# Optimization experiments

Measured on AMD Instinct MI355X. Metric: run time of the kernel, lower is better.

Reference implementation:

```python
import jax, jax.numpy as jnp
import numpy as np

CUTOFF = 5.0
MAX_NBR = 32      # max_num_neighbors
LOOP = True
B, M = 128, 1024  # molecules, atoms per molecule (batch is uniform: batch[i] = i // M)
BOX = 26.0        # box side chosen so ~30 atoms fall within CUTOFF


def setup_inputs() -> dict:
    key = jax.random.key(0)
    pos = jax.random.uniform(key, (B * M, 3), dtype=jnp.float32) * BOX
    batch = jnp.repeat(jnp.arange(B, dtype=jnp.int32), M)
    return {"pos": pos, "batch": batch}


def reference(pos, batch):
    # radius_graph with per-graph (molecule) candidate search. Equal-size
    # molecules (batch = arange // M) let us use a dense [B, M, M] candidate
    # matrix per molecule; truncation keeps the K nearest within cutoff
    # (PyG keeps an arbitrary K within cutoff; nearest-K is the deterministic
    # variant). Output has fixed shape [2, B*M*K] padded with self-loops.
    posb = pos.reshape(B, M, 3)
    sq = jnp.sum(posb * posb, axis=-1)                       # [B, M]
    dot = jnp.einsum('bmd,bnd->bmn', posb, posb)             # [B, M, M]
    d2 = jnp.maximum(sq[:, :, None] + sq[:, None, :] - 2.0 * dot, 0.0)
    within = d2 <= CUTOFF * CUTOFF
    if not LOOP:
        within = within & ~jnp.eye(M, dtype=bool)[None]
    neg = jnp.where(within, -d2, -jnp.inf)
    vals, idx = jax.lax.top_k(neg, MAX_NBR)                  # [B, M, K]
    valid = jnp.isfinite(vals)
    center = jnp.arange(M, dtype=idx.dtype)[None, :, None]   # [1, M, 1]
    idx_eff = jnp.where(valid, idx, center)                  # pad invalid -> self

    b_ix = jnp.arange(B)[:, None, None]
    nbr = posb[b_ix, idx_eff]                                # [B, M, K, 3]
    edge_vec = nbr - posb[:, :, None, :]                     # pos[src] - pos[dst]

    is_self = idx_eff == center
    wmask = valid & ~is_self                                 # self-loops get weight 0
    d2sel = jnp.sum(edge_vec * edge_vec, axis=-1)
    edge_weight = jnp.where(wmask, jnp.sqrt(jnp.where(wmask, d2sel, 1.0)), 0.0)

    offs = (jnp.arange(B, dtype=idx.dtype) * M)[:, None, None]
    src = (offs + idx_eff).reshape(-1)                       # neighbor (edge_index[0])
    dst = jnp.broadcast_to(offs + center, (B, M, MAX_NBR)).reshape(-1)
    edge_index = jnp.stack([src, dst])                       # [2, B*M*K]
    return edge_index, edge_weight.reshape(-1), edge_vec.reshape(-1, 3)
```

## Files before the change

kernel.cpp:

```cpp
#include <hip/hip_runtime.h>

#define NB 128
#define NM 1024
#define NK 32
#define NS 12
#define CUT2 25.0f
#define CUT2_BITS 0x41C80000u
#define KEYMASK   0xFFFFFC00u
#define INV_CELL  (1.0f/5.2f)
#define NCELL3    125

typedef unsigned int   u32;
typedef unsigned short u16;
typedef float vf4 __attribute__((ext_vector_type(4)));

__global__ __launch_bounds__(256) void pack_bin(const float* __restrict__ pos,
                                                float4* __restrict__ sortedg,
                                                u16* __restrict__ origid,
                                                u16* __restrict__ startsg)
{
  __shared__ u32 hist[NCELL3 + 1];
  __shared__ u32 starts[NCELL3 + 1];
  __shared__ u32 cur[NCELL3];
  const int tid = threadIdx.x;
  const int mb  = blockIdx.x;
  if (tid <= NCELL3) hist[tid] = 0;
  __syncthreads();

  float xx[4], yy[4], zz[4];
  int cid[4];
#pragma unroll
  for (int k = 0; k < 4; ++k) {
    int i  = k * 256 + tid;
    int gi = mb * NM + i;
    float x = pos[3*gi+0], y = pos[3*gi+1], z = pos[3*gi+2];
    xx[k] = x; yy[k] = y; zz[k] = z;
    int cx = (int)(x * INV_CELL); cx = cx > 4 ? 4 : cx;
    int cy = (int)(y * INV_CELL); cy = cy > 4 ? 4 : cy;
    int cz = (int)(z * INV_CELL); cz = cz > 4 ? 4 : cz;
    cid[k] = (cz * 5 + cy) * 5 + cx;
    atomicAdd(&hist[cid[k]], 1u);
  }
  __syncthreads();
  if (tid == 0) {
    u32 run = 0;
    for (int i = 0; i < NCELL3; ++i) { starts[i] = run; run += hist[i]; }
    starts[NCELL3] = run;
  }
  __syncthreads();
  if (tid <= NCELL3) startsg[mb*(NCELL3+1) + tid] = (u16)starts[tid];
  if (tid <  NCELL3) cur[tid] = starts[tid];
  __syncthreads();
#pragma unroll
  for (int k = 0; k < 4; ++k) {
    int i = k * 256 + tid;
    u32 p = atomicAdd(&cur[cid[k]], 1u);
    float x = xx[k], y = yy[k], z = zz[k];
    sortedg[mb*NM + p] = make_float4(-2.f*x, -2.f*y, -2.f*z, x*x + y*y + z*z);
    origid[mb*NM + p]  = (u16)i;
  }
}

__device__ __forceinline__ void ce_asc(u32 &a, u32 &b) {
  u32 mn = a < b ? a : b;
  u32 mx = a < b ? b : a;
  a = mn; b = mx;
}

template <int N, int K, int D>
__device__ __forceinline__ void bitonic_pass(u32* r) {
#pragma unroll
  for (int i = 0; i < N; ++i)
    if ((i & D) == 0) {
      if ((i & K) == 0) ce_asc(r[i], r[i | D]);
      else              ce_asc(r[i | D], r[i]);
    }
}

__global__ __launch_bounds__(256, 8) void radius_knn(const float4* __restrict__ sortedg,
                                                     const u16* __restrict__ origg,
                                                     const u16* __restrict__ startsg,
                                                     float* __restrict__ out)
{
  __shared__ u32 lmem[4096];
  __shared__ u16 orig_s[NM];
  u16* lists  = (u16*)lmem;
  u32* rowbuf = lmem + 1536;
  u16* flat   = (u16*)(lmem + 1568);
  u16* st_s   = (u16*)(lmem + 2112);

  const int tid     = threadIdx.x;
  const int ctr     = tid & 63;
  const int quarter = tid >> 6;
  const int molb    = blockIdx.x & 127;
  const int grp     = blockIdx.x >> 7;
  const int spos    = grp * 64 + ctr;
  const int molbase = molb * NM;

  for (int t = tid; t < NM; t += 256) orig_s[t] = origg[molbase + t];
  if (tid <= NCELL3) st_s[tid] = startsg[molb*(NCELL3+1) + tid];

  const float4 mc  = sortedg[molbase + spos];
  const int   mloc = origg[molbase + spos];
  const float mex = -0.5f*mc.x, mey = -0.5f*mc.y, mez = -0.5f*mc.z;
  const float mew = mc.w;
  const int c = molbase + mloc;

  int cx = (int)(mex * INV_CELL); cx = cx > 4 ? 4 : cx;
  int cy = (int)(mey * INV_CELL); cy = cy > 4 ? 4 : cy;
  int cz = (int)(mez * INV_CELL); cz = cz > 4 ? 4 : cz;
  int mnx = cx, mxx = cx, mny = cy, mxy = cy, mnz = cz, mxz = cz;
#pragma unroll
  for (int m = 32; m; m >>= 1) {
    mnx = min(mnx, __shfl_xor(mnx, m, 64)); mxx = max(mxx, __shfl_xor(mxx, m, 64));
    mny = min(mny, __shfl_xor(mny, m, 64)); mxy = max(mxy, __shfl_xor(mxy, m, 64));
    mnz = min(mnz, __shfl_xor(mnz, m, 64)); mxz = max(mxz, __shfl_xor(mxz, m, 64));
  }
  __syncthreads();

  if (quarter == 0) {
    const int zlo = max(mnz-1, 0), zhi = min(mxz+1, 4);
    const int ylo = max(mny-1, 0), yhi = min(mxy+1, 4);
    const int xlo = max(mnx-1, 0), xhi = min(mxx+1, 4);
    const int rz = ctr / 5, ry = ctr % 5;
    int czc = zlo + rz, cyc = ylo + ry;
    u32 rs = 0, len = 0;
    if (ctr < 25 && czc <= zhi && cyc <= yhi) {
      int rowb = (czc*5 + cyc)*5;
      rs  = st_s[rowb + xlo];
      u32 re = st_s[rowb + xhi + 1];
      len = re - rs;
    }
    u32 incl = len;
#pragma unroll
    for (int d = 1; d < 32; d <<= 1) {
      u32 t = __shfl_up(incl, d, 64);
      if (ctr >= d) incl += t;
    }
    if (ctr < 25)  rowbuf[ctr] = (rs << 16) | (incl - len);
    if (ctr == 24) { rowbuf[25] = incl; lmem[1563] = incl; }
  }
  __syncthreads();

  const int C  = (int)lmem[1563];
  const int C4 = (C + 15) & ~15;
  for (int p = tid; p < C; p += 256) {
    int r = 0;
    while (p >= (int)(rowbuf[r+1] & 0xFFFFu)) ++r;
    u32 e = rowbuf[r];
    int j = (int)(e >> 16) + (p - (int)(e & 0xFFFFu));
    flat[(p & 3) * 264 + (p >> 2)] = (u16)j;
  }
  for (int p = C + tid; p < C4; p += 256) flat[(p & 3) * 264 + (p >> 2)] = 0xFFFFu;
  __syncthreads();

  int cnt = 0;
  const u16* fl = flat + quarter * 264;
  const int T = C4 >> 4;
  for (int g = 0; g < T; ++g) {
    uint2 jj = *((const uint2*)(fl + 4*g));
    int j0 = jj.x & 0xFFFF, j1 = jj.x >> 16;
    int j2 = jj.y & 0xFFFF, j3 = jj.y >> 16;
    float4 c0 = sortedg[molbase + (j0 & 1023)];
    float4 c1 = sortedg[molbase + (j1 & 1023)];
    float4 c2 = sortedg[molbase + (j2 & 1023)];
    float4 c3 = sortedg[molbase + (j3 & 1023)];
#define PROC(cj, jv)                                                        \
    {                                                                       \
      float d2 = __builtin_fmaf(mex, cj.x, __builtin_fmaf(mey, cj.y,        \
                 __builtin_fmaf(mez, cj.z, mew + cj.w)));                   \
      d2 = (jv < 1024) ? d2 : 1.0e30f;                       \
      int slot = cnt < NS ? cnt : (NS - 1);                                 \
      lists[slot * 256 + tid] = (u16)(jv & 1023);                           \
      cnt += (d2 <= CUT2) ? 1 : 0;                                          \
    }
    PROC(c0, j0) PROC(c1, j1) PROC(c2, j2) PROC(c3, j3)
#undef PROC
  }
  if (cnt > NS) cnt = NS;

  const u32 PADK = 0x7F800000u | (u32)spos;
  u32 r[32];
#pragma unroll
  for (int k = 0; k < 16; ++k) {
    u32 key = PADK;
    if (k < cnt) {
      int j = lists[k * 256 + tid];
      float4 cj = sortedg[molbase + j];
      float d2 = fmaxf(__builtin_fmaf(mex, cj.x,
                  __builtin_fmaf(mey, cj.y,
                  __builtin_fmaf(mez, cj.z, mew + cj.w))), 0.f);
      key = (__float_as_uint(d2) & KEYMASK) | (u32)j;
    }
    r[k] = key;
  }
  bitonic_pass<16, 2, 1>(r);
  bitonic_pass<16, 4, 2>(r); bitonic_pass<16, 4, 1>(r);
  bitonic_pass<16, 8, 4>(r); bitonic_pass<16, 8, 2>(r); bitonic_pass<16, 8, 1>(r);
  bitonic_pass<16,16, 8>(r); bitonic_pass<16,16, 4>(r); bitonic_pass<16,16, 2>(r); bitonic_pass<16,16, 1>(r);

  __syncthreads();
  {
    u32* myp = lmem + quarter * 1024 + ctr * 16;
#pragma unroll
    for (int k = 0; k < 16; ++k) myp[(k + ctr) & 15] = r[k];
  }
  __syncthreads();
  {
    u32* op = lmem + (quarter ^ 1) * 1024 + ctr * 16;
#pragma unroll
    for (int i = 0; i < 16; ++i) r[16 + i] = op[((15 - i) + ctr) & 15];
  }
  bitonic_pass<32,32,16>(r); bitonic_pass<32,32, 8>(r); bitonic_pass<32,32, 4>(r);
  bitonic_pass<32,32, 2>(r); bitonic_pass<32,32, 1>(r);

  __syncthreads();
  const int pairId = quarter >> 1;
  if ((quarter & 1) == 0) {
    u32* pp = lmem + pairId * 2048 + ctr * 32;
#pragma unroll
    for (int k = 0; k < 32; ++k) pp[(k + ctr) & 31] = r[k];
  }
  __syncthreads();
  {
    u32* opp = lmem + (1 - pairId) * 2048 + ctr * 32;
#pragma unroll
    for (int t = 0; t < 32; ++t) {
      u32 v = opp[((31 - t) + ctr) & 31];
      r[t] = r[t] < v ? r[t] : v;
    }
  }
  bitonic_pass<32,32,16>(r); bitonic_pass<32,32, 8>(r); bitonic_pass<32,32, 4>(r);
  bitonic_pass<32,32, 2>(r); bitonic_pass<32,32, 1>(r);

  const long long E = (long long)NB * NM * NK;
  const float base = (float)molbase;
  const float nmex = -mex, nmey = -mey, nmez = -mez;

  if (quarter == 0) {
    vf4* ps = (vf4*)(out       + (size_t)c * NK);
    vf4* pd = (vf4*)(out +   E + (size_t)c * NK);
    const float fc = (float)c;
    const vf4 dstv = {fc, fc, fc, fc};
#pragma unroll
    for (int q = 0; q < 8; ++q) {
      float sv[4];
#pragma unroll
      for (int u = 0; u < 4; ++u) {
        int idx = (int)(r[4*q + u] & 1023u);
        sv[u] = base + (float)orig_s[idx];
      }
      ps[q] = (vf4){sv[0], sv[1], sv[2], sv[3]};
      pd[q] = dstv;
    }
  } else if (quarter == 1) {
    vf4* pw = (vf4*)(out + 2*E + (size_t)c * NK);
#pragma unroll
    for (int q = 0; q < 8; ++q) {
      float wv[4];
#pragma unroll
      for (int u = 0; u < 4; ++u) {
        u32 key = r[4*q + u];
        int idx = (int)(key & 1023u);
        float4 cj = sortedg[molbase + idx];
        bool valid = (key & KEYMASK) <= CUT2_BITS;
        float vx = __builtin_fmaf(-0.5f, cj.x, nmex);
        float vy = __builtin_fmaf(-0.5f, cj.y, nmey);
        float vz = __builtin_fmaf(-0.5f, cj.z, nmez);
        bool wm  = valid && (idx != spos);
        float d2s = vx*vx + vy*vy + vz*vz;
        wv[u] = wm ? sqrtf(d2s) : 0.0f;
      }
      pw[q] = (vf4){wv[0], wv[1], wv[2], wv[3]};
    }
  } else if (quarter == 2) {
    vf4* pv = (vf4*)(out + 3*E + (size_t)c * NK * 3);
#pragma unroll
    for (int q = 0; q < 4; ++q) {
      float vv[12];
#pragma unroll
      for (int u = 0; u < 4; ++u) {
        int idx = (int)(r[4*q + u] & 1023u);
        float4 cj = sortedg[molbase + idx];
        vv[3*u+0] = __builtin_fmaf(-0.5f, cj.x, nmex);
        vv[3*u+1] = __builtin_fmaf(-0.5f, cj.y, nmey);
        vv[3*u+2] = __builtin_fmaf(-0.5f, cj.z, nmez);
      }
      pv[3*q+0] = (vf4){vv[0], vv[1], vv[2],  vv[3]};
      pv[3*q+1] = (vf4){vv[4], vv[5], vv[6],  vv[7]};
      pv[3*q+2] = (vf4){vv[8], vv[9], vv[10], vv[11]};
    }
  } else {
    vf4* pv = (vf4*)(out + 3*E + (size_t)c * NK * 3) + 12;
#pragma unroll
    for (int q = 0; q < 4; ++q) {
      float vv[12];
#pragma unroll
      for (int u = 0; u < 4; ++u) {
        int idx = (int)(r[16 + 4*q + u] & 1023u);
        float4 cj = sortedg[molbase + idx];
        vv[3*u+0] = __builtin_fmaf(-0.5f, cj.x, nmex);
        vv[3*u+1] = __builtin_fmaf(-0.5f, cj.y, nmey);
        vv[3*u+2] = __builtin_fmaf(-0.5f, cj.z, nmez);
      }
      pv[3*q+0] = (vf4){vv[0], vv[1], vv[2],  vv[3]};
      pv[3*q+1] = (vf4){vv[4], vv[5], vv[6],  vv[7]};
      pv[3*q+2] = (vf4){vv[8], vv[9], vv[10], vv[11]};
    }
  }
}

extern "C" void kernel_launch(void* const* d_in, const int* in_sizes, int n_in,
                              void* d_out, int out_size, void* d_ws, size_t ws_size,
                              hipStream_t stream) {
  const float* pos = (const float*)d_in[0];
  float* out = (float*)d_out;
  float4* sortedg = (float4*)d_ws;
  u16* origid  = (u16*)((char*)d_ws + (size_t)(2u << 20));
  u16* startsg = (u16*)((char*)d_ws + (size_t)(2u << 20) + (256u << 10));
  hipLaunchKernelGGL(pack_bin, dim3(NB), dim3(256), 0, stream,
                     pos, sortedg, origid, startsg);
  hipLaunchKernelGGL(radius_knn, dim3(NB * (NM / 64)), dim3(256), 0, stream,
                     sortedg, origid, startsg, out);
}
```

Before: 193.2 us.

## Split neighbor selection from edge emission via compact key buffer and inverse permutation

The kNN kernel now stores a compact 16-bit key list per atom (index plus validity bit) to workspace, and a new emit_edges kernel writes all outputs in original atom order using an inverse permutation built in pack_bin. The aim is coalesced, row-ordered output writes instead of scattered writes by sorted order, and less divergent per-quarter tail work. The cost is an extra kernel launch and a round trip of the key buffer through global memory. The split path runs only when the workspace is large enough, with the fused kernel kept as a fallback.

```diff
diff --git a/kernel.cpp b/kernel.cpp
--- a/kernel.cpp
+++ b/kernel.cpp
@@ -10,6 +10,12 @@
 #define INV_CELL  (1.0f/5.2f)
 #define NCELL3    125
 
+#define OFF_ORIG   (2u << 20)
+#define OFF_STARTS (OFF_ORIG + (256u << 10))
+#define OFF_INV    (OFF_STARTS + (32u << 10))
+#define OFF_KEYS   (OFF_INV + (256u << 10))
+#define WS_NEEDED  (OFF_KEYS + (size_t)NB * NM * NK * 2)
+
 typedef unsigned int   u32;
 typedef unsigned short u16;
 typedef float vf4 __attribute__((ext_vector_type(4)));
@@ -17,6 +23,7 @@
 __global__ __launch_bounds__(256) void pack_bin(const float* __restrict__ pos,
                                                 float4* __restrict__ sortedg,
                                                 u16* __restrict__ origid,
+                                                u16* __restrict__ invpos,
                                                 u16* __restrict__ startsg)
 {
   __shared__ u32 hist[NCELL3 + 1];
@@ -58,6 +65,7 @@
     float x = xx[k], y = yy[k], z = zz[k];
     sortedg[mb*NM + p] = make_float4(-2.f*x, -2.f*y, -2.f*z, x*x + y*y + z*z);
     origid[mb*NM + p]  = (u16)i;
+    invpos[mb*NM + i]  = (u16)p;
   }
 }
 
@@ -77,9 +85,11 @@
     }
 }
 
+template <bool SPLIT>
 __global__ __launch_bounds__(256, 8) void radius_knn(const float4* __restrict__ sortedg,
                                                      const u16* __restrict__ origg,
                                                      const u16* __restrict__ startsg,
+                                                     u16* __restrict__ keys,
                                                      float* __restrict__ out)
 {
   __shared__ u32 lmem[4096];
@@ -97,14 +107,13 @@
   const int spos    = grp * 64 + ctr;
   const int molbase = molb * NM;
 
-  for (int t = tid; t < NM; t += 256) orig_s[t] = origg[molbase + t];
+  if constexpr (!SPLIT)
+    for (int t = tid; t < NM; t += 256) orig_s[t] = origg[molbase + t];
   if (tid <= NCELL3) st_s[tid] = startsg[molb*(NCELL3+1) + tid];
 
   const float4 mc  = sortedg[molbase + spos];
-  const int   mloc = origg[molbase + spos];
   const float mex = -0.5f*mc.x, mey = -0.5f*mc.y, mez = -0.5f*mc.z;
   const float mew = mc.w;
-  const int c = molbase + mloc;
 
   int cx = (int)(mex * INV_CELL); cx = cx > 4 ? 4 : cx;
   int cy = (int)(mey * INV_CELL); cy = cy > 4 ? 4 : cy;
@@ -206,13 +215,13 @@
     for (int k = 0; k < 16; ++k) myp[(k + ctr) & 15] = r[k];
   }
   __syncthreads();
-  {
+  if (!SPLIT || (quarter & 1) == 0) {
     u32* op = lmem + (quarter ^ 1) * 1024 + ctr * 16;
 #pragma unroll
     for (int i = 0; i < 16; ++i) r[16 + i] = op[((15 - i) + ctr) & 15];
-  }
-  bitonic_pass<32,32,16>(r); bitonic_pass<32,32, 8>(r); bitonic_pass<32,32, 4>(r);
-  bitonic_pass<32,32, 2>(r); bitonic_pass<32,32, 1>(r);
+    bitonic_pass<32,32,16>(r); bitonic_pass<32,32, 8>(r); bitonic_pass<32,32, 4>(r);
+    bitonic_pass<32,32, 2>(r); bitonic_pass<32,32, 1>(r);
+  }
 
   __syncthreads();
   const int pairId = quarter >> 1;
@@ -222,91 +231,169 @@
     for (int k = 0; k < 32; ++k) pp[(k + ctr) & 31] = r[k];
   }
   __syncthreads();
-  {
+  if (!SPLIT || quarter == 0) {
     u32* opp = lmem + (1 - pairId) * 2048 + ctr * 32;
 #pragma unroll
     for (int t = 0; t < 32; ++t) {
       u32 v = opp[((31 - t) + ctr) & 31];
       r[t] = r[t] < v ? r[t] : v;
     }
-  }
-  bitonic_pass<32,32,16>(r); bitonic_pass<32,32, 8>(r); bitonic_pass<32,32, 4>(r);
-  bitonic_pass<32,32, 2>(r); bitonic_pass<32,32, 1>(r);
-
+    bitonic_pass<32,32,16>(r); bitonic_pass<32,32, 8>(r); bitonic_pass<32,32, 4>(r);
+    bitonic_pass<32,32, 2>(r); bitonic_pass<32,32, 1>(r);
+  }
+
+  if constexpr (SPLIT) {
+    if (quarter == 0) {
+      u32 pk[16];
+#pragma unroll
+      for (int i = 0; i < 16; ++i) {
+        u32 klo = r[2*i], khi = r[2*i+1];
+        u32 plo = (((klo & KEYMASK) <= CUT2_BITS) ? 1024u : 0u) | (klo & 1023u);
+        u32 phi = (((khi & KEYMASK) <= CUT2_BITS) ? 1024u : 0u) | (khi & 1023u);
+        pk[i] = plo | (phi << 16);
+      }
+      uint4* kp = (uint4*)(keys + (size_t)(molbase + spos) * 32);
+#pragma unroll
+      for (int i = 0; i < 4; ++i)
+        kp[i] = make_uint4(pk[4*i], pk[4*i+1], pk[4*i+2], pk[4*i+3]);
+    }
+    return;
+  } else {
+    const int mloc = orig_s[spos];
+    const int c = molbase + mloc;
+    const long long E = (long long)NB * NM * NK;
+    const float base = (float)molbase;
+    const float nmex = -mex, nmey = -mey, nmez = -mez;
+
+    if (quarter == 0) {
+      vf4* ps = (vf4*)(out       + (size_t)c * NK);
+      vf4* pd = (vf4*)(out +   E + (size_t)c * NK);
+      const float fc = (float)c;
+      const vf4 dstv = {fc, fc, fc, fc};
+#pragma unroll
+      for (int q = 0; q < 8; ++q) {
+        float sv[4];
+#pragma unroll
+        for (int u = 0; u < 4; ++u) {
+          int idx = (int)(r[4*q + u] & 1023u);
+          sv[u] = base + (float)orig_s[idx];
+        }
+        ps[q] = (vf4){sv[0], sv[1], sv[2], sv[3]};
+        pd[q] = dstv;
+      }
+    } else if (quarter == 1) {
+      vf4* pw = (vf4*)(out + 2*E + (size_t)c * NK);
+#pragma unroll
+      for (int q = 0; q < 8; ++q) {
+        float wv[4];
+#pragma unroll
+        for (int u = 0; u < 4; ++u) {
+          u32 key = r[4*q + u];
+          int idx = (int)(key & 1023u);
+          float4 cj = sortedg[molbase + idx];
+          bool valid = (key & KEYMASK) <= CUT2_BITS;
+          float vx = __builtin_fmaf(-0.5f, cj.x, nmex);
+          float vy = __builtin_fmaf(-0.5f, cj.y, nmey);
+          float vz = __builtin_fmaf(-0.5f, cj.z, nmez);
+          bool wm  = valid && (idx != spos);
+          float d2s = vx*vx + vy*vy + vz*vz;
+          wv[u] = wm ? sqrtf(d2s) : 0.0f;
+        }
+        pw[q] = (vf4){wv[0], wv[1], wv[2], wv[3]};
+      }
+    } else if (quarter == 2) {
+      vf4* pv = (vf4*)(out + 3*E + (size_t)c * NK * 3);
+#pragma unroll
+      for (int q = 0; q < 4; ++q) {
+        float vv[12];
+#pragma unroll
+        for (int u = 0; u < 4; ++u) {
+          int idx = (int)(r[4*q + u] & 1023u);
+          float4 cj = sortedg[molbase + idx];
+          vv[3*u+0] = __builtin_fmaf(-0.5f, cj.x, nmex);
+          vv[3*u+1] = __builtin_fmaf(-0.5f, cj.y, nmey);
+          vv[3*u+2] = __builtin_fmaf(-0.5f, cj.z, nmez);
+        }
+        pv[3*q+0] = (vf4){vv[0], vv[1], vv[2],  vv[3]};
+        pv[3*q+1] = (vf4){vv[4], vv[5], vv[6],  vv[7]};
+        pv[3*q+2] = (vf4){vv[8], vv[9], vv[10], vv[11]};
+      }
+    } else {
+      vf4* pv = (vf4*)(out + 3*E + (size_t)c * NK * 3) + 12;
+#pragma unroll
+      for (int q = 0; q < 4; ++q) {
+        float vv[12];
+#pragma unroll
+        for (int u = 0; u < 4; ++u) {
+          int idx = (int)(r[16 + 4*q + u] & 1023u);
+          float4 cj = sortedg[molbase + idx];
+          vv[3*u+0] = __builtin_fmaf(-0.5f, cj.x, nmex);
+          vv[3*u+1] = __builtin_fmaf(-0.5f, cj.y, nmey);
+          vv[3*u+2] = __builtin_fmaf(-0.5f, cj.z, nmez);
+        }
+        pv[3*q+0] = (vf4){vv[0], vv[1], vv[2],  vv[3]};
+        pv[3*q+1] = (vf4){vv[4], vv[5], vv[6],  vv[7]};
+        pv[3*q+2] = (vf4){vv[8], vv[9], vv[10], vv[11]};
+      }
+    }
+  }
+}
+
+__global__ __launch_bounds__(256) void emit_edges(const float4* __restrict__ sortedg,
+                                                  const u16* __restrict__ origg,
+                                                  const u16* __restrict__ invpos,
+                                                  const u16* __restrict__ keys,
+                                                  float* __restrict__ out)
+{
+  const int r  = blockIdx.x * 256 + threadIdx.x;
+  const int mb = r >> 10;
+  const int molbase = mb << 10;
+  const int spos = invpos[r];
+  const float4 mc = sortedg[molbase + spos];
+  const float mex = -0.5f*mc.x, mey = -0.5f*mc.y, mez = -0.5f*mc.z;
+  const float nmex = -mex, nmey = -mey, nmez = -mez;
   const long long E = (long long)NB * NM * NK;
   const float base = (float)molbase;
-  const float nmex = -mex, nmey = -mey, nmez = -mez;
-
-  if (quarter == 0) {
-    vf4* ps = (vf4*)(out       + (size_t)c * NK);
-    vf4* pd = (vf4*)(out +   E + (size_t)c * NK);
-    const float fc = (float)c;
-    const vf4 dstv = {fc, fc, fc, fc};
-#pragma unroll
-    for (int q = 0; q < 8; ++q) {
-      float sv[4];
-#pragma unroll
-      for (int u = 0; u < 4; ++u) {
-        int idx = (int)(r[4*q + u] & 1023u);
-        sv[u] = base + (float)orig_s[idx];
-      }
-      ps[q] = (vf4){sv[0], sv[1], sv[2], sv[3]};
-      pd[q] = dstv;
-    }
-  } else if (quarter == 1) {
-    vf4* pw = (vf4*)(out + 2*E + (size_t)c * NK);
-#pragma unroll
-    for (int q = 0; q < 8; ++q) {
-      float wv[4];
-#pragma unroll
-      for (int u = 0; u < 4; ++u) {
-        u32 key = r[4*q + u];
-        int idx = (int)(key & 1023u);
-        float4 cj = sortedg[molbase + idx];
-        bool valid = (key & KEYMASK) <= CUT2_BITS;
-        float vx = __builtin_fmaf(-0.5f, cj.x, nmex);
-        float vy = __builtin_fmaf(-0.5f, cj.y, nmey);
-        float vz = __builtin_fmaf(-0.5f, cj.z, nmez);
-        bool wm  = valid && (idx != spos);
-        float d2s = vx*vx + vy*vy + vz*vz;
-        wv[u] = wm ? sqrtf(d2s) : 0.0f;
-      }
-      pw[q] = (vf4){wv[0], wv[1], wv[2], wv[3]};
-    }
-  } else if (quarter == 2) {
-    vf4* pv = (vf4*)(out + 3*E + (size_t)c * NK * 3);
-#pragma unroll
-    for (int q = 0; q < 4; ++q) {
-      float vv[12];
-#pragma unroll
-      for (int u = 0; u < 4; ++u) {
-        int idx = (int)(r[4*q + u] & 1023u);
-        float4 cj = sortedg[molbase + idx];
-        vv[3*u+0] = __builtin_fmaf(-0.5f, cj.x, nmex);
-        vv[3*u+1] = __builtin_fmaf(-0.5f, cj.y, nmey);
-        vv[3*u+2] = __builtin_fmaf(-0.5f, cj.z, nmez);
-      }
-      pv[3*q+0] = (vf4){vv[0], vv[1], vv[2],  vv[3]};
-      pv[3*q+1] = (vf4){vv[4], vv[5], vv[6],  vv[7]};
-      pv[3*q+2] = (vf4){vv[8], vv[9], vv[10], vv[11]};
-    }
-  } else {
-    vf4* pv = (vf4*)(out + 3*E + (size_t)c * NK * 3) + 12;
-#pragma unroll
-    for (int q = 0; q < 4; ++q) {
-      float vv[12];
-#pragma unroll
-      for (int u = 0; u < 4; ++u) {
-        int idx = (int)(r[16 + 4*q + u] & 1023u);
-        float4 cj = sortedg[molbase + idx];
-        vv[3*u+0] = __builtin_fmaf(-0.5f, cj.x, nmex);
-        vv[3*u+1] = __builtin_fmaf(-0.5f, cj.y, nmey);
-        vv[3*u+2] = __builtin_fmaf(-0.5f, cj.z, nmez);
-      }
-      pv[3*q+0] = (vf4){vv[0], vv[1], vv[2],  vv[3]};
-      pv[3*q+1] = (vf4){vv[4], vv[5], vv[6],  vv[7]};
-      pv[3*q+2] = (vf4){vv[8], vv[9], vv[10], vv[11]};
-    }
+
+  const uint4* kp = (const uint4*)(keys + (size_t)(molbase + spos) * 32);
+  u32 wds[16];
+#pragma unroll
+  for (int i = 0; i < 4; ++i) {
+    uint4 kv = kp[i];
+    wds[4*i+0] = kv.x; wds[4*i+1] = kv.y; wds[4*i+2] = kv.z; wds[4*i+3] = kv.w;
+  }
+
+  vf4* ps = (vf4*)(out       + (size_t)r * NK);
+  vf4* pd = (vf4*)(out +   E + (size_t)r * NK);
+  vf4* pw = (vf4*)(out + 2*E + (size_t)r * NK);
+  vf4* pv = (vf4*)(out + 3*E + (size_t)r * NK * 3);
+  const float fr = (float)r;
+  const vf4 dstv = {fr, fr, fr, fr};
+
+#pragma unroll
+  for (int q = 0; q < 8; ++q) {
+    float sv[4], wv[4], vvv[12];
+#pragma unroll
+    for (int u = 0; u < 4; ++u) {
+      u32 key = (wds[2*q + (u >> 1)] >> ((u & 1) * 16)) & 0xFFFFu;
+      int idx = (int)(key & 1023u);
+      bool valid = (key & 1024u) != 0;
+      float4 cj = sortedg[molbase + idx];
+      float vx = __builtin_fmaf(-0.5f, cj.x, nmex);
+      float vy = __builtin_fmaf(-0.5f, cj.y, nmey);
+      float vz = __builtin_fmaf(-0.5f, cj.z, nmez);
+      bool wm  = valid && (idx != spos);
+      float d2s = vx*vx + vy*vy + vz*vz;
+      wv[u] = wm ? sqrtf(d2s) : 0.0f;
+      sv[u] = base + (float)origg[molbase + idx];
+      vvv[3*u+0] = vx; vvv[3*u+1] = vy; vvv[3*u+2] = vz;
+    }
+    ps[q] = (vf4){sv[0], sv[1], sv[2], sv[3]};
+    pd[q] = dstv;
+    pw[q] = (vf4){wv[0], wv[1], wv[2], wv[3]};
+    pv[3*q+0] = (vf4){vvv[0], vvv[1], vvv[2],  vvv[3]};
+    pv[3*q+1] = (vf4){vvv[4], vvv[5], vvv[6],  vvv[7]};
+    pv[3*q+2] = (vf4){vvv[8], vvv[9], vvv[10], vvv[11]};
   }
 }
 
@@ -316,10 +403,20 @@
   const float* pos = (const float*)d_in[0];
   float* out = (float*)d_out;
   float4* sortedg = (float4*)d_ws;
-  u16* origid  = (u16*)((char*)d_ws + (size_t)(2u << 20));
-  u16* startsg = (u16*)((char*)d_ws + (size_t)(2u << 20) + (256u << 10));
+  u16* origid  = (u16*)((char*)d_ws + OFF_ORIG);
+  u16* startsg = (u16*)((char*)d_ws + OFF_STARTS);
+  u16* invpos  = (u16*)((char*)d_ws + OFF_INV);
+  u16* keys    = (u16*)((char*)d_ws + OFF_KEYS);
+
   hipLaunchKernelGGL(pack_bin, dim3(NB), dim3(256), 0, stream,
-                     pos, sortedg, origid, startsg);
-  hipLaunchKernelGGL(radius_knn, dim3(NB * (NM / 64)), dim3(256), 0, stream,
-                     sortedg, origid, startsg, out);
-}
+                     pos, sortedg, origid, invpos, startsg);
+  if (ws_size >= WS_NEEDED) {
+    hipLaunchKernelGGL((radius_knn<true>), dim3(NB * (NM / 64)), dim3(256), 0, stream,
+                       sortedg, origid, startsg, keys, out);
+    hipLaunchKernelGGL(emit_edges, dim3((NB * NM) / 256), dim3(256), 0, stream,
+                       sortedg, origid, invpos, keys, out);
+  } else {
+    hipLaunchKernelGGL((radius_knn<false>), dim3(NB * (NM / 64)), dim3(256), 0, stream,
+                       sortedg, origid, startsg, keys, out);
+  }
+}
```

New measurement: 232.4 us. +20.3%, slower.
